# Optimization experiments

Hardware: AMD Instinct MI355X
Metric: run time of the kernel (lower is better)

The kernel has to match this reference:

```python
import jax, jax.numpy as jnp
import numpy as np

N_NODES = 50000
N_EDGES = 800000
D_IN = 128
D_HID = 128
D_OUT = 128


def setup_inputs() -> dict:
    key = jax.random.key(0)
    ks = jax.random.split(key, 10)
    x = jax.random.normal(ks[0], (N_NODES, D_IN), dtype=jnp.float32)
    edge_index = jax.random.randint(ks[1], (2, N_EDGES), 0, N_NODES, dtype=jnp.int64)
    edge_index_inter = jax.random.randint(ks[2], (2, N_EDGES), 0, N_NODES, dtype=jnp.int64)
    # nn.Linear-style params: W [out, in], b [out]
    def linear(k, fan_in, fan_out):
        k1, k2 = jax.random.split(k)
        bound = 1.0 / np.sqrt(fan_in)
        W = jax.random.uniform(k1, (fan_out, fan_in), minval=-bound, maxval=bound, dtype=jnp.float32)
        b = jax.random.uniform(k2, (fan_out,), minval=-bound, maxval=bound, dtype=jnp.float32)
        return W, b
    W1, b1 = linear(ks[3], D_IN, D_HID)
    W2, b2 = linear(ks[4], D_HID, D_HID)
    W3, b3 = linear(ks[5], D_HID, D_OUT)
    return {"x": x, "W1": W1, "b1": b1, "W2": W2, "b2": b2, "W3": W3, "b3": b3,
            "edge_index": edge_index, "edge_index_inter": edge_index_inter}


def _gnn_layer(h, W, b, src, dst, n_nodes):
    # message: lin(x_j - x_i); x_j = source features, x_i = target features (PyG convention)
    msg = (h[src] - h[dst]) @ W.T + b          # [E, out]
    # aggr='add': scatter-add messages into target nodes
    return jax.ops.segment_sum(msg, dst, num_segments=n_nodes)  # [N, out]


def reference(x, W1, b1, W2, b2, W3, b3, edge_index, edge_index_inter):
    src, dst = edge_index[0], edge_index[1]
    n = x.shape[0]
    h = _gnn_layer(x, W1, b1, src, dst, n)
    h = _gnn_layer(h, W2, b2, src, dst, n)
    return _gnn_layer(h, W3, b3, src, dst, n)
```

## Files before the change

### kernel.cpp

```cpp
#include <hip/hip_runtime.h>

#define N_NODES 50000
#define N_EDGES 800000
#define D 128
#define TN 16
#define TSTR 136
#define SCAN_BLOCKS 196

typedef __attribute__((ext_vector_type(8))) short bf16x8;
typedef __attribute__((ext_vector_type(4))) float f32x4;

__device__ __forceinline__ unsigned short f32_to_bf16_rne(float f) {
    unsigned u = __float_as_uint(f);
    u += 0x7fffu + ((u >> 16) & 1u);
    return (unsigned short)(u >> 16);
}

__device__ __forceinline__ void acc_bf16x4(uint2 r, float& x, float& y, float& z, float& w) {
    x += __uint_as_float(r.x << 16);
    y += __uint_as_float(r.x & 0xffff0000u);
    z += __uint_as_float(r.y << 16);
    w += __uint_as_float(r.y & 0xffff0000u);
}

template <int U>
__device__ __forceinline__ void gather_phase(const unsigned short* __restrict__ hb,
                                             int myidx, int i, int sub, int q,
                                             float* ax, float* ay, float* az, float* aw) {
    int si[U];
    uint2 rr[U];
#pragma unroll
    for (int u = 0; u < U; ++u) si[u] = __shfl(myidx, i + 2 * u + sub, 64);
#pragma unroll
    for (int u = 0; u < U; ++u) rr[u] = *(const uint2*)(hb + (size_t)si[u] * D + 4 * q);
#pragma unroll
    for (int u = 0; u < U; ++u)
        acc_bf16x4(rr[u], ax[u & 3], ay[u & 3], az[u & 3], aw[u & 3]);
}

__global__ void prep_kernel(const int* __restrict__ dst, int* __restrict__ counts,
                            int* __restrict__ rank,
                            const float* __restrict__ x, unsigned short* __restrict__ xb) {
    const int t = blockIdx.x * blockDim.x + threadIdx.x;
    if (t < N_EDGES) {
        rank[t] = atomicAdd(&counts[dst[t]], 1);
    }
    {
        const float4 v0 = *(const float4*)(x + (size_t)t * 8);
        const float4 v1 = *(const float4*)(x + (size_t)t * 8 + 4);
        uint4 p;
        p.x = (unsigned)f32_to_bf16_rne(v0.x) | ((unsigned)f32_to_bf16_rne(v0.y) << 16);
        p.y = (unsigned)f32_to_bf16_rne(v0.z) | ((unsigned)f32_to_bf16_rne(v0.w) << 16);
        p.z = (unsigned)f32_to_bf16_rne(v1.x) | ((unsigned)f32_to_bf16_rne(v1.y) << 16);
        p.w = (unsigned)f32_to_bf16_rne(v1.z) | ((unsigned)f32_to_bf16_rne(v1.w) << 16);
        *(uint4*)(xb + (size_t)t * 8) = p;
    }
}

__global__ void block_sum_kernel(const int* __restrict__ counts, int* __restrict__ bsum) {
    __shared__ int red[256];
    const int tid = threadIdx.x;
    const int i = blockIdx.x * 256 + tid;
    red[tid] = (i < N_NODES) ? counts[i] : 0;
    __syncthreads();
    for (int s = 128; s > 0; s >>= 1) {
        if (tid < s) red[tid] += red[tid + s];
        __syncthreads();
    }
    if (tid == 0) bsum[blockIdx.x] = red[0];
}

__global__ void bsum_scan_kernel(const int* __restrict__ bsum,
                                 int* __restrict__ bpre,
                                 int* __restrict__ offsets) {
    __shared__ int s[256];
    const int tid = threadIdx.x;
    const int v = (tid < SCAN_BLOCKS) ? bsum[tid] : 0;
    s[tid] = v;
    __syncthreads();
    for (int off = 1; off < 256; off <<= 1) {
        int a = (tid >= off) ? s[tid - off] : 0;
        __syncthreads();
        s[tid] += a;
        __syncthreads();
    }
    bpre[tid] = s[tid] - v;
    if (tid == 255) offsets[N_NODES] = s[255];
}

__global__ void offsets_wfrag_kernel(const int* __restrict__ counts,
                                     const int* __restrict__ bpre,
                                     int* __restrict__ offsets,
                                     const float* __restrict__ W1,
                                     const float* __restrict__ W2,
                                     const float* __restrict__ W3,
                                     unsigned short* __restrict__ Wb) {
    if (blockIdx.x < SCAN_BLOCKS) {
        __shared__ int s[256];
        const int tid = threadIdx.x;
        const int i = blockIdx.x * 256 + tid;
        const int v = (i < N_NODES) ? counts[i] : 0;
        s[tid] = v;
        __syncthreads();
        for (int off = 1; off < 256; off <<= 1) {
            int a = (tid >= off) ? s[tid - off] : 0;
            __syncthreads();
            s[tid] += a;
            __syncthreads();
        }
        const int excl = s[tid] - v + bpre[blockIdx.x];
        if (i < N_NODES) offsets[i] = excl;
    } else {
        const int unit = (blockIdx.x - SCAN_BLOCKS) * 2 + (threadIdx.x >> 7);
        const int w = unit >> 7;
        const int o = unit & 127;
        const int k = threadIdx.x & 127;
        const float* W = (w == 0) ? W1 : (w == 1) ? W2 : W3;
        const unsigned short v = f32_to_bf16_rne(W[o * D + k]);
        const int nt = o >> 4, n = o & 15;
        const int kc = k >> 5, kr = k & 31, quad = kr >> 3, j = kr & 7;
        const int lane = quad * 16 + n;
        Wb[(((size_t)w * 8 + nt) * 4 + kc) * 512 + lane * 8 + j] = v;
    }
}

__global__ void fill_kernel(const int* __restrict__ src, const int* __restrict__ dst,
                            const int* __restrict__ rank,
                            const int* __restrict__ offsets, int* __restrict__ esrc) {
    int e = blockIdx.x * blockDim.x + threadIdx.x;
    if (e < N_EDGES) {
        esrc[offsets[dst[e]] + rank[e]] = src[e];
    }
}

template <bool OUT_BF16>
__global__ __launch_bounds__(256) void gnn_layer_kernel(
    const unsigned short* __restrict__ hb,
    const int* __restrict__ offsets,
    const int* __restrict__ esrc,
    const unsigned short* __restrict__ Wb,
    const float* __restrict__ bias,
    float* __restrict__ outf,
    unsigned short* __restrict__ outb) {

    __shared__ __align__(16) unsigned short tb[TN][TSTR];
    __shared__ float degf[TN];

    const int tid = threadIdx.x;
    const int wave = tid >> 6;
    const int lane = tid & 63;
    const int sub = lane >> 5;
    const int q = lane & 31;
    const int vbase = blockIdx.x * TN;

    for (int j = wave * 4; j < wave * 4 + 4; ++j) {
        const int v = vbase + j;
        const int beg = offsets[v];
        const int deg = offsets[v + 1] - beg;

        float ax[4] = {0.f, 0.f, 0.f, 0.f};
        float ay[4] = {0.f, 0.f, 0.f, 0.f};
        float az[4] = {0.f, 0.f, 0.f, 0.f};
        float aw[4] = {0.f, 0.f, 0.f, 0.f};

        for (int base = 0; base < deg; base += 64) {
            const int cnt = min(deg - base, 64);
            int myidx = 0;
            if (lane < cnt) myidx = esrc[beg + base + lane];

            int i = 0;
            for (; i + 16 <= cnt; i += 16)
                gather_phase<8>(hb, myidx, i, sub, q, ax, ay, az, aw);
            if (i + 8 <= cnt) {
                gather_phase<4>(hb, myidx, i, sub, q, ax, ay, az, aw);
                i += 8;
            }
            if (i + 4 <= cnt) {
                gather_phase<2>(hb, myidx, i, sub, q, ax, ay, az, aw);
                i += 4;
            }
            if (i + 2 <= cnt) {
                gather_phase<1>(hb, myidx, i, sub, q, ax, ay, az, aw);
                i += 2;
            }
            if (i < cnt) {
                const int s0 = __shfl(myidx, i, 64);
                if (sub == 0) {
                    const uint2 r = *(const uint2*)(hb + (size_t)s0 * D + 4 * q);
                    acc_bf16x4(r, ax[0], ay[0], az[0], aw[0]);
                }
            }
        }

        float sx = (ax[0] + ax[1]) + (ax[2] + ax[3]);
        float sy = (ay[0] + ay[1]) + (ay[2] + ay[3]);
        float sz = (az[0] + az[1]) + (az[2] + az[3]);
        float sw = (aw[0] + aw[1]) + (aw[2] + aw[3]);

        sx += __shfl_xor(sx, 32, 64);
        sy += __shfl_xor(sy, 32, 64);
        sz += __shfl_xor(sz, 32, 64);
        sw += __shfl_xor(sw, 32, 64);

        const float dv = (float)deg;
        if (sub == 0) {
            const uint2 r = *(const uint2*)(hb + (size_t)v * D + 4 * q);
            const float tx = sx - dv * __uint_as_float(r.x << 16);
            const float ty = sy - dv * __uint_as_float(r.x & 0xffff0000u);
            const float tz = sz - dv * __uint_as_float(r.y << 16);
            const float tw = sw - dv * __uint_as_float(r.y & 0xffff0000u);
            unsigned p0 = (unsigned)f32_to_bf16_rne(tx) | ((unsigned)f32_to_bf16_rne(ty) << 16);
            unsigned p1 = (unsigned)f32_to_bf16_rne(tz) | ((unsigned)f32_to_bf16_rne(tw) << 16);
            *(uint2*)&tb[j][4 * q] = make_uint2(p0, p1);
        }
        if (lane == 0) degf[j] = dv;
    }
    __syncthreads();

    const int n16 = lane & 15;
    const int quad = lane >> 4;

    bf16x8 afrag[4];
#pragma unroll
    for (int kc = 0; kc < 4; ++kc)
        afrag[kc] = *(const bf16x8*)&tb[n16][kc * 32 + quad * 8];

#pragma unroll
    for (int i = 0; i < 2; ++i) {
        const int nt = wave * 2 + i;
        f32x4 acc = {0.f, 0.f, 0.f, 0.f};
#pragma unroll
        for (int kc = 0; kc < 4; ++kc) {
            const bf16x8 bfrag = *(const bf16x8*)&Wb[((nt * 4 + kc) * 64 + lane) * 8];
            acc = __builtin_amdgcn_mfma_f32_16x16x32_bf16(afrag[kc], bfrag, acc, 0, 0, 0);
        }
        const int o = nt * 16 + n16;
        const float bo = bias[o];
#pragma unroll
        for (int r = 0; r < 4; ++r) {
            const int m = quad * 4 + r;
            const float val = acc[r] + degf[m] * bo;
            if (OUT_BF16)
                outb[(size_t)(vbase + m) * D + o] = f32_to_bf16_rne(val);
            else
                outf[(size_t)(vbase + m) * D + o] = val;
        }
    }
}

extern "C" void kernel_launch(void* const* d_in, const int* in_sizes, int n_in,
                              void* d_out, int out_size, void* d_ws, size_t ws_size,
                              hipStream_t stream) {
    const float* x  = (const float*)d_in[0];
    const float* W1 = (const float*)d_in[1];
    const float* b1 = (const float*)d_in[2];
    const float* W2 = (const float*)d_in[3];
    const float* b2 = (const float*)d_in[4];
    const float* W3 = (const float*)d_in[5];
    const float* b3 = (const float*)d_in[6];
    const int*   ei = (const int*)d_in[7];

    const int* src = ei;
    const int* dst = ei + N_EDGES;
    float* out = (float*)d_out;

    char* ws = (char*)d_ws;
    int* counts  = (int*)ws;                      ws += 204800;
    int* offsets = (int*)ws;                      ws += 204800;
    int* bsum    = (int*)ws;                      ws += 1024;
    int* bpre    = (int*)ws;                      ws += 1024;
    int* rank    = (int*)ws;                      ws += (size_t)N_EDGES * 4;
    int* esrc    = (int*)ws;                      ws += (size_t)N_EDGES * 4;
    unsigned short* Wb = (unsigned short*)ws;     ws += 3 * 16384 * 2;
    unsigned short* xb = (unsigned short*)ws;     ws += (size_t)N_NODES * D * 2;
    unsigned short* h1 = (unsigned short*)ws;     ws += (size_t)N_NODES * D * 2;
    unsigned short* h2 = (unsigned short*)ws;

    hipMemsetAsync(counts, 0, N_NODES * sizeof(int), stream);
    prep_kernel<<<(N_EDGES + 255) / 256, 256, 0, stream>>>(dst, counts, rank, x, xb);
    block_sum_kernel<<<SCAN_BLOCKS, 256, 0, stream>>>(counts, bsum);
    bsum_scan_kernel<<<1, 256, 0, stream>>>(bsum, bpre, offsets);
    offsets_wfrag_kernel<<<SCAN_BLOCKS + 192, 256, 0, stream>>>(counts, bpre, offsets,
                                                                W1, W2, W3, Wb);
    fill_kernel<<<(N_EDGES + 255) / 256, 256, 0, stream>>>(src, dst, rank, offsets, esrc);

    const int blocks = N_NODES / TN;

    gnn_layer_kernel<true ><<<blocks, 256, 0, stream>>>(xb, offsets, esrc, Wb,          b1, nullptr, h1);
    gnn_layer_kernel<true ><<<blocks, 256, 0, stream>>>(h1, offsets, esrc, Wb + 16384,  b2, nullptr, h2);
    gnn_layer_kernel<false><<<blocks, 256, 0, stream>>>(h2, offsets, esrc, Wb + 32768,  b3, out, nullptr);
}
```

Measured before the change: 272.0 us.

## Fuse CSR build preprocessing into one cooperative kernel with grid syncs

Replaces the memset and five separate preprocessing launches (counting, block sums, scan, offsets plus weight packing, fill) with a single cooperative kernel that uses grid-wide syncs between phases. This removes launch overhead and inter-kernel gaps. In exchange each phase runs with a fixed grid of 1024 blocks, which requires all blocks to be co-resident. The grid syncs also add their own cost, and the later phases leave most blocks idle.

```diff
diff --git a/kernel.cpp b/kernel.cpp
--- a/kernel.cpp
+++ b/kernel.cpp
@@ -1,4 +1,7 @@
 #include <hip/hip_runtime.h>
+#include <hip/hip_cooperative_groups.h>
+
+namespace cg = cooperative_groups;
 
 #define N_NODES 50000
 #define N_EDGES 800000
@@ -6,6 +9,7 @@
 #define TN 16
 #define TSTR 136
 #define SCAN_BLOCKS 196
+#define COOP_BLOCKS 1024
 
 typedef __attribute__((ext_vector_type(8))) short bf16x8;
 typedef __attribute__((ext_vector_type(4))) float f32x4;
@@ -38,14 +42,30 @@
         acc_bf16x4(rr[u], ax[u & 3], ay[u & 3], az[u & 3], aw[u & 3]);
 }
 
-__global__ void prep_kernel(const int* __restrict__ dst, int* __restrict__ counts,
-                            int* __restrict__ rank,
-                            const float* __restrict__ x, unsigned short* __restrict__ xb) {
-    const int t = blockIdx.x * blockDim.x + threadIdx.x;
-    if (t < N_EDGES) {
-        rank[t] = atomicAdd(&counts[dst[t]], 1);
-    }
-    {
+__global__ __launch_bounds__(256) void csr_coop_kernel(
+    const int* __restrict__ src, const int* __restrict__ dst,
+    const float* __restrict__ x,
+    const float* __restrict__ W1, const float* __restrict__ W2,
+    const float* __restrict__ W3,
+    int* __restrict__ counts, int* __restrict__ rank,
+    int* __restrict__ offsets, int* __restrict__ bsum, int* __restrict__ bpre,
+    int* __restrict__ esrc,
+    unsigned short* __restrict__ Wb, unsigned short* __restrict__ xb) {
+
+    cg::grid_group grid = cg::this_grid();
+    __shared__ int s[256];
+
+    const int tid = threadIdx.x;
+    const int gtid = blockIdx.x * 256 + tid;
+    const int GT = COOP_BLOCKS * 256;
+
+    for (int i = gtid; i < N_NODES; i += GT) counts[i] = 0;
+    grid.sync();
+
+    for (int e = gtid; e < N_EDGES; e += GT)
+        rank[e] = atomicAdd(&counts[dst[e]], 1);
+
+    for (int t = gtid; t < N_NODES * D / 8; t += GT) {
         const float4 v0 = *(const float4*)(x + (size_t)t * 8);
         const float4 v1 = *(const float4*)(x + (size_t)t * 8 + 4);
         uint4 p;
@@ -55,49 +75,48 @@
         p.w = (unsigned)f32_to_bf16_rne(v1.z) | ((unsigned)f32_to_bf16_rne(v1.w) << 16);
         *(uint4*)(xb + (size_t)t * 8) = p;
     }
-}
-
-__global__ void block_sum_kernel(const int* __restrict__ counts, int* __restrict__ bsum) {
-    __shared__ int red[256];
-    const int tid = threadIdx.x;
-    const int i = blockIdx.x * 256 + tid;
-    red[tid] = (i < N_NODES) ? counts[i] : 0;
-    __syncthreads();
-    for (int s = 128; s > 0; s >>= 1) {
-        if (tid < s) red[tid] += red[tid + s];
+
+    if (gtid < 3 * D * D) {
+        const int w = gtid >> 14;
+        const int o = (gtid >> 7) & 127;
+        const int k = gtid & 127;
+        const float* W = (w == 0) ? W1 : (w == 1) ? W2 : W3;
+        const unsigned short v = f32_to_bf16_rne(W[o * D + k]);
+        const int nt = o >> 4, n = o & 15;
+        const int kc = k >> 5, kr = k & 31, quad = kr >> 3, j = kr & 7;
+        const int lane = quad * 16 + n;
+        Wb[(((size_t)w * 8 + nt) * 4 + kc) * 512 + lane * 8 + j] = v;
+    }
+    grid.sync();
+
+    if (blockIdx.x < SCAN_BLOCKS) {
+        const int i = blockIdx.x * 256 + tid;
+        s[tid] = (i < N_NODES) ? counts[i] : 0;
         __syncthreads();
-    }
-    if (tid == 0) bsum[blockIdx.x] = red[0];
-}
-
-__global__ void bsum_scan_kernel(const int* __restrict__ bsum,
-                                 int* __restrict__ bpre,
-                                 int* __restrict__ offsets) {
-    __shared__ int s[256];
-    const int tid = threadIdx.x;
-    const int v = (tid < SCAN_BLOCKS) ? bsum[tid] : 0;
-    s[tid] = v;
-    __syncthreads();
-    for (int off = 1; off < 256; off <<= 1) {
-        int a = (tid >= off) ? s[tid - off] : 0;
+        for (int st = 128; st > 0; st >>= 1) {
+            if (tid < st) s[tid] += s[tid + st];
+            __syncthreads();
+        }
+        if (tid == 0) bsum[blockIdx.x] = s[0];
+    }
+    grid.sync();
+
+    if (blockIdx.x == 0) {
+        const int v = (tid < SCAN_BLOCKS) ? bsum[tid] : 0;
+        s[tid] = v;
         __syncthreads();
-        s[tid] += a;
-        __syncthreads();
-    }
-    bpre[tid] = s[tid] - v;
-    if (tid == 255) offsets[N_NODES] = s[255];
-}
-
-__global__ void offsets_wfrag_kernel(const int* __restrict__ counts,
-                                     const int* __restrict__ bpre,
-                                     int* __restrict__ offsets,
-                                     const float* __restrict__ W1,
-                                     const float* __restrict__ W2,
-                                     const float* __restrict__ W3,
-                                     unsigned short* __restrict__ Wb) {
+        for (int off = 1; off < 256; off <<= 1) {
+            int a = (tid >= off) ? s[tid - off] : 0;
+            __syncthreads();
+            s[tid] += a;
+            __syncthreads();
+        }
+        bpre[tid] = s[tid] - v;
+        if (tid == 255) offsets[N_NODES] = s[255];
+    }
+    grid.sync();
+
     if (blockIdx.x < SCAN_BLOCKS) {
-        __shared__ int s[256];
-        const int tid = threadIdx.x;
         const int i = blockIdx.x * 256 + tid;
         const int v = (i < N_NODES) ? counts[i] : 0;
         s[tid] = v;
@@ -110,27 +129,11 @@
         }
         const int excl = s[tid] - v + bpre[blockIdx.x];
         if (i < N_NODES) offsets[i] = excl;
-    } else {
-        const int unit = (blockIdx.x - SCAN_BLOCKS) * 2 + (threadIdx.x >> 7);
-        const int w = unit >> 7;
-        const int o = unit & 127;
-        const int k = threadIdx.x & 127;
-        const float* W = (w == 0) ? W1 : (w == 1) ? W2 : W3;
-        const unsigned short v = f32_to_bf16_rne(W[o * D + k]);
-        const int nt = o >> 4, n = o & 15;
-        const int kc = k >> 5, kr = k & 31, quad = kr >> 3, j = kr & 7;
-        const int lane = quad * 16 + n;
-        Wb[(((size_t)w * 8 + nt) * 4 + kc) * 512 + lane * 8 + j] = v;
-    }
-}
-
-__global__ void fill_kernel(const int* __restrict__ src, const int* __restrict__ dst,
-                            const int* __restrict__ rank,
-                            const int* __restrict__ offsets, int* __restrict__ esrc) {
-    int e = blockIdx.x * blockDim.x + threadIdx.x;
-    if (e < N_EDGES) {
+    }
+    grid.sync();
+
+    for (int e = gtid; e < N_EDGES; e += GT)
         esrc[offsets[dst[e]] + rank[e]] = src[e];
-    }
 }
 
 template <bool OUT_BF16>
@@ -276,13 +279,17 @@
     unsigned short* h1 = (unsigned short*)ws;     ws += (size_t)N_NODES * D * 2;
     unsigned short* h2 = (unsigned short*)ws;
 
-    hipMemsetAsync(counts, 0, N_NODES * sizeof(int), stream);
-    prep_kernel<<<(N_EDGES + 255) / 256, 256, 0, stream>>>(dst, counts, rank, x, xb);
-    block_sum_kernel<<<SCAN_BLOCKS, 256, 0, stream>>>(counts, bsum);
-    bsum_scan_kernel<<<1, 256, 0, stream>>>(bsum, bpre, offsets);
-    offsets_wfrag_kernel<<<SCAN_BLOCKS + 192, 256, 0, stream>>>(counts, bpre, offsets,
-                                                                W1, W2, W3, Wb);
-    fill_kernel<<<(N_EDGES + 255) / 256, 256, 0, stream>>>(src, dst, rank, offsets, esrc);
+    {
+        void* args[] = {
+            (void*)&src, (void*)&dst, (void*)&x,
+            (void*)&W1, (void*)&W2, (void*)&W3,
+            (void*)&counts, (void*)&rank, (void*)&offsets,
+            (void*)&bsum, (void*)&bpre, (void*)&esrc,
+            (void*)&Wb, (void*)&xb
+        };
+        hipLaunchCooperativeKernel((const void*)csr_coop_kernel,
+                                   dim3(COOP_BLOCKS), dim3(256), args, 0, stream);
+    }
 
     const int blocks = N_NODES / TN;
 
```

Measured after the change: 773.8 us. 2.84x slower.
